# Optimization experiments

Measured on AMD Instinct MI355X. Metric: run time of the kernel, lower is better.

Reference implementation:

```python
import jax, jax.numpy as jnp
import numpy as np

N0, N1, N2 = 400000, 75000, 15000
E1, E2 = 1200000, 240000
F_IN, NC = 64, 40
H1, C1 = 2, 8          # layer 1: heads=2, out_channels=8 -> concat dim 16
H2, C2 = 1, NC         # layer 2: heads=1, out_channels=num_classes
NEG_SLOPE = 0.2


def gat_conv(x_src, x_dst, src, dst, Ws, Wd, att_s, att_d, bias, heads, ch):
    """PyG GATConv on bipartite (x_src, x_dst) with remove+add self loops."""
    n_dst = x_dst.shape[0]
    hs = (x_src @ Ws).reshape(-1, heads, ch)   # [N_src, H, C]
    hd = (x_dst @ Wd).reshape(-1, heads, ch)   # [N_dst, H, C]
    a_s = (hs * att_s).sum(-1)                 # [N_src, H]
    a_d = (hd * att_d).sum(-1)                 # [N_dst, H]
    loops = jnp.arange(n_dst)
    src_all = jnp.concatenate([src, loops])
    dst_all = jnp.concatenate([dst, loops])
    # remove_self_loops: drop pre-existing i->i edges; add_self_loops: appended
    valid = jnp.concatenate([src != dst, jnp.ones(n_dst, dtype=bool)])[:, None]
    logits = jax.nn.leaky_relu(a_s[src_all] + a_d[dst_all], NEG_SLOPE)  # [E, H]
    logits = jnp.where(valid, logits, -jnp.inf)
    m = jax.ops.segment_max(logits, dst_all, num_segments=n_dst)        # [N_dst, H]
    w = jnp.where(valid, jnp.exp(logits - m[dst_all]), 0.0)
    denom = jax.ops.segment_sum(w, dst_all, num_segments=n_dst)
    alpha = w / denom[dst_all]                                          # [E, H]
    out = jax.ops.segment_sum(alpha[:, :, None] * hs[src_all], dst_all,
                              num_segments=n_dst)                       # [N_dst, H, C]
    return out.reshape(n_dst, heads * ch) + bias


def setup_inputs() -> dict:
    key = jax.random.key(0)
    ks = jax.random.split(key, 16)
    s = 0.1
    return {
        "x": jax.random.normal(ks[0], (N0, F_IN), dtype=jnp.float32),
        "e1_src": jax.random.randint(ks[1], (E1,), 0, N0),
        "e1_dst": jax.random.randint(ks[2], (E1,), 0, N1),
        "e2_src": jax.random.randint(ks[3], (E2,), 0, N1),
        "e2_dst": jax.random.randint(ks[4], (E2,), 0, N2),
        "W1s": jax.random.normal(ks[5], (F_IN, H1 * C1), dtype=jnp.float32) * s,
        "W1d": jax.random.normal(ks[6], (F_IN, H1 * C1), dtype=jnp.float32) * s,
        "att1_s": jax.random.normal(ks[7], (H1, C1), dtype=jnp.float32) * s,
        "att1_d": jax.random.normal(ks[8], (H1, C1), dtype=jnp.float32) * s,
        "b1": jnp.zeros((H1 * C1,), dtype=jnp.float32),
        "W2s": jax.random.normal(ks[9], (H1 * C1, H2 * C2), dtype=jnp.float32) * s,
        "W2d": jax.random.normal(ks[10], (H1 * C1, H2 * C2), dtype=jnp.float32) * s,
        "att2_s": jax.random.normal(ks[11], (H2, C2), dtype=jnp.float32) * s,
        "att2_d": jax.random.normal(ks[12], (H2, C2), dtype=jnp.float32) * s,
        "b2": jnp.zeros((H2 * C2,), dtype=jnp.float32),
    }


def reference(x, e1_src, e1_dst, e2_src, e2_dst,
              W1s, W1d, att1_s, att1_d, b1,
              W2s, W2d, att2_s, att2_d, b2):
    h = gat_conv(x, x[:N1], e1_src, e1_dst, W1s, W1d, att1_s, att1_d, b1, H1, C1)
    h = jax.nn.elu(h)
    o = gat_conv(h, h[:N2], e2_src, e2_dst, W2s, W2d, att2_s, att2_d, b2, H2, C2)
    return jax.nn.log_softmax(o, axis=-1)
```

## Files before the change

### kernel.cpp

```cpp
#include <hip/hip_runtime.h>
#include <hip/hip_bf16.h>

constexpr int N0 = 400000, N1 = 75000, N2 = 15000;
constexpr int E1 = 1200000, E2 = 240000;
constexpr int NC = 40;
constexpr float NEG_SLOPE = 0.2f;

constexpr int BK1 = 128;
constexpr int NB1 = (N1 + BK1 - 1) / BK1;
constexpr int CAPB1 = 2432;
constexpr int BK2 = 32;
constexpr int NB2 = (N2 + BK2 - 1) / BK2;
constexpr int CAPB2 = 704;

constexpr int TILE = 8192;
constexpr int NT1 = (E1 + TILE - 1) / TILE;
constexpr int NT2 = (E2 + TILE - 1) / TILE;
constexpr int BPJ = (N0 + 511) / 512;

__device__ __forceinline__ float leaky(float v) { return v > 0.f ? v : NEG_SLOPE * v; }

__device__ __forceinline__ unsigned bf16pair(float lo, float hi) {
    unsigned a = __float_as_uint(lo), b = __float_as_uint(hi);
    a = (a + 0x7FFFu + ((a >> 16) & 1u)) >> 16;
    b = (b + 0x7FFFu + ((b >> 16) & 1u)) & 0xFFFF0000u;
    return a | b;
}
__device__ __forceinline__ float bfLo(unsigned w) { return __uint_as_float(w << 16); }
__device__ __forceinline__ float bfHi(unsigned w) { return __uint_as_float(w & 0xFFFF0000u); }

__global__ __launch_bounds__(512, 4) void k1_kernel(
    const float* __restrict__ x,
    const float* __restrict__ W1s, const float* __restrict__ W1d,
    const float* __restrict__ att1s, const float* __restrict__ att1d,
    const int* __restrict__ e1s, const int* __restrict__ e1d,
    const int* __restrict__ e2s, const int* __restrict__ e2d,
    unsigned* __restrict__ rec1, float* __restrict__ a_d1,
    int* __restrict__ gcnt1, unsigned* __restrict__ bin1,
    int* __restrict__ gcnt2, unsigned* __restrict__ bin2)
{
    __shared__ int hist[NB1];
    __shared__ int gbase[NB1];

    int bid = blockIdx.x;
    if (bid < BPJ) {
        int node = bid * 512 + threadIdx.x;
        if (node >= N0) return;
        const float4* xp = (const float4*)(x + (size_t)node * 64);
        float4 xr[16];
        #pragma unroll
        for (int j = 0; j < 16; ++j) xr[j] = xp[j];

        float ss[16];
        #pragma unroll
        for (int c = 0; c < 16; ++c) ss[c] = 0.f;
        #pragma unroll
        for (int j = 0; j < 16; ++j) {
            float xk[4] = {xr[j].x, xr[j].y, xr[j].z, xr[j].w};
            #pragma unroll
            for (int kk = 0; kk < 4; ++kk)
                #pragma unroll
                for (int c = 0; c < 16; ++c)
                    ss[c] = fmaf(xk[kk], W1s[(4 * j + kk) * 16 + c], ss[c]);
        }
        float a0 = 0.f, a1 = 0.f;
        #pragma unroll
        for (int c = 0; c < 8; ++c) {
            a0 = fmaf(ss[c], att1s[c], a0);
            a1 = fmaf(ss[8 + c], att1s[8 + c], a1);
        }
        unsigned* rp = rec1 + (size_t)node * 16;
        ((uint4*)rp)[0] = make_uint4(bf16pair(ss[0], ss[1]), bf16pair(ss[2], ss[3]),
                                     bf16pair(ss[4], ss[5]), bf16pair(ss[6], ss[7]));
        ((uint4*)rp)[1] = make_uint4(bf16pair(ss[8], ss[9]), bf16pair(ss[10], ss[11]),
                                     bf16pair(ss[12], ss[13]), bf16pair(ss[14], ss[15]));
        ((uint4*)rp)[2] = make_uint4(__float_as_uint(a0), __float_as_uint(a1), 0u, 0u);
        ((uint4*)rp)[3] = make_uint4(0u, 0u, 0u, 0u);

        if (node < N1) {
            float sd[16];
            #pragma unroll
            for (int c = 0; c < 16; ++c) sd[c] = 0.f;
            #pragma unroll
            for (int j = 0; j < 16; ++j) {
                float xk[4] = {xr[j].x, xr[j].y, xr[j].z, xr[j].w};
                #pragma unroll
                for (int kk = 0; kk < 4; ++kk)
                    #pragma unroll
                    for (int c = 0; c < 16; ++c)
                        sd[c] = fmaf(xk[kk], W1d[(4 * j + kk) * 16 + c], sd[c]);
            }
            float d0 = 0.f, d1 = 0.f;
            #pragma unroll
            for (int c = 0; c < 8; ++c) {
                d0 = fmaf(sd[c], att1d[c], d0);
                d1 = fmaf(sd[8 + c], att1d[8 + c], d1);
            }
            ((float2*)a_d1)[node] = make_float2(d0, d1);
        }
        return;
    }
    bid -= BPJ;
    const bool isL1 = bid < NT1;
    const int* es = isL1 ? e1s : e2s;
    const int* ed = isL1 ? e1d : e2d;
    const int nE = isL1 ? E1 : E2;
    const int nb = isL1 ? NB1 : NB2;
    const int cap = isL1 ? CAPB1 : CAPB2;
    const int shift = isL1 ? 7 : 5;
    const int lsh = isL1 ? 19 : 17;
    int* gc = isL1 ? gcnt1 : gcnt2;
    unsigned* gbin = isL1 ? bin1 : bin2;
    const int base = (isL1 ? bid : bid - NT1) * TILE;
    const int lim = min(TILE, nE - base);

    for (int b = threadIdx.x; b < nb; b += 512) hist[b] = 0;
    __syncthreads();
    for (int i = threadIdx.x; i < lim; i += 512) {
        int s = es[base + i], d = ed[base + i];
        if (s != d) atomicAdd(&hist[d >> shift], 1);
    }
    __syncthreads();
    for (int b = threadIdx.x; b < nb; b += 512) {
        int c = hist[b];
        gbase[b] = (c > 0) ? atomicAdd(&gc[b], c) : 0;
        hist[b] = 0;
    }
    __syncthreads();
    for (int i = threadIdx.x; i < lim; i += 512) {
        int s = es[base + i], d = ed[base + i];
        if (s != d) {
            int b = d >> shift;
            int pos = gbase[b] + atomicAdd(&hist[b], 1);
            if (pos < cap)
                gbin[(size_t)b * cap + pos] =
                    (unsigned)s | ((unsigned)(d & ((1 << shift) - 1)) << lsh);
        }
    }
}

__global__ __launch_bounds__(512) void k2_kernel(
    const int* __restrict__ gcnt1, const unsigned* __restrict__ bin1,
    const unsigned* __restrict__ rec1, const float* __restrict__ a_d1,
    const float* __restrict__ b1,
    const float* __restrict__ W2s, const float* __restrict__ W2d,
    const float* __restrict__ att2s, const float* __restrict__ att2d,
    unsigned* __restrict__ rec2)
{
    __shared__ unsigned srt[CAPB1];
    __shared__ int hist[BK1], start[BK1 + 1];
    __shared__ float w2sl[640], va[16], vd[16];
    __shared__ float h1s[BK1][17];

    const int b = blockIdx.x, tid = threadIdx.x;
    const int d0 = b * BK1;
    const int nN = min(BK1, N1 - d0);
    const int ncnt = min(gcnt1[b], CAPB1);
    const unsigned* bp = bin1 + (size_t)b * CAPB1;

    for (int i = tid; i < 640; i += 512) w2sl[i] = W2s[i];
    if (tid < BK1) hist[tid] = 0;
    if (tid >= 128 && tid < 144) {
        int k = tid - 128;
        float sa = 0.f, sd = 0.f;
        for (int cc = 0; cc < 40; ++cc) {
            sa = fmaf(W2s[k * 40 + cc], att2s[cc], sa);
            sd = fmaf(W2d[k * 40 + cc], att2d[cc], sd);
        }
        va[k] = sa; vd[k] = sd;
    }
    __syncthreads();
    for (int i = tid; i < ncnt; i += 512) atomicAdd(&hist[bp[i] >> 19], 1);
    __syncthreads();
    if (tid == 0) {
        int a = 0;
        for (int k = 0; k < BK1; ++k) { start[k] = a; a += hist[k]; }
        start[BK1] = a;
    }
    __syncthreads();
    if (tid < BK1) hist[tid] = start[tid];
    __syncthreads();
    for (int i = tid; i < ncnt; i += 512) {
        unsigned p = bp[i];
        int pos = atomicAdd(&hist[p >> 19], 1);
        srt[pos] = p & 0x7FFFFu;
    }
    __syncthreads();

    const int g = tid >> 4, c = tid & 15, h = c >> 3;
    const int wbase = tid & 48;
    const int wmap = (c < 8) ? c : (8 + ((c >> 2) & 1));
    for (int n = g; n < nN; n += 32) {
        const int node = d0 + n;
        const float ad = a_d1[(size_t)node * 2 + h];
        const int st = start[n], cnt = start[n + 1] - start[n];
        unsigned rwA = rec1[(size_t)node * 16 + wmap];
        unsigned rwB = (cnt > 0) ? rec1[(size_t)srt[st] * 16 + wmap] : 0u;
        float accv = 0.f, den = 0.f;
        for (int j = 0; j <= cnt; ++j) {
            unsigned rwC = (j + 2 <= cnt) ? rec1[(size_t)srt[st + j + 1] * 16 + wmap] : 0u;
            float asv = __uint_as_float((unsigned)__shfl((int)rwA, wbase + 8 + 4 * h, 64));
            unsigned chw = (unsigned)__shfl((int)rwA, wbase + (c >> 1), 64);
            float hv = (c & 1) ? bfHi(chw) : bfLo(chw);
            float w = __expf(leaky(asv + ad));
            accv = fmaf(w, hv, accv);
            den += w;
            rwA = rwB; rwB = rwC;
        }
        float v = accv / den + b1[c];
        h1s[n][c] = v > 0.f ? v : (__expf(v) - 1.f);
    }
    __syncthreads();
    for (int i = tid; i < nN * 24; i += 512) {
        int nn = i / 24, w = i - nn * 24;
        unsigned* rp = rec2 + (size_t)(d0 + nn) * 24;
        if (w < 20) {
            int c0 = 2 * w, c1 = c0 + 1;
            float s0 = 0.f, s1 = 0.f;
            #pragma unroll
            for (int k = 0; k < 16; ++k) {
                float hk = h1s[nn][k];
                s0 = fmaf(hk, w2sl[k * 40 + c0], s0);
                s1 = fmaf(hk, w2sl[k * 40 + c1], s1);
            }
            rp[w] = bf16pair(s0, s1);
        } else if (w < 22) {
            const float* vv = (w == 20) ? va : vd;
            float s = 0.f;
            #pragma unroll
            for (int k = 0; k < 16; ++k) s = fmaf(h1s[nn][k], vv[k], s);
            rp[w] = __float_as_uint(s);
        }
    }
}

__global__ __launch_bounds__(1024) void k3_kernel(
    const int* __restrict__ gcnt2, const unsigned* __restrict__ bin2,
    const unsigned* __restrict__ rec2, const float* __restrict__ b2,
    float* __restrict__ out)
{
    __shared__ unsigned srt[CAPB2];
    __shared__ int hist[BK2], start[BK2 + 1];

    const int b = blockIdx.x, tid = threadIdx.x;
    const int d0 = b * BK2;
    const int nN = min(BK2, N2 - d0);
    const int ncnt = min(gcnt2[b], CAPB2);
    const unsigned* bp = bin2 + (size_t)b * CAPB2;

    if (tid < BK2) hist[tid] = 0;
    __syncthreads();
    for (int i = tid; i < ncnt; i += 1024) atomicAdd(&hist[bp[i] >> 17], 1);
    __syncthreads();
    if (tid == 0) {
        int a = 0;
        for (int k = 0; k < BK2; ++k) { start[k] = a; a += hist[k]; }
        start[BK2] = a;
    }
    __syncthreads();
    if (tid < BK2) hist[tid] = start[tid];
    __syncthreads();
    for (int i = tid; i < ncnt; i += 1024) {
        unsigned p = bp[i];
        int pos = atomicAdd(&hist[p >> 17], 1);
        srt[pos] = p & 0x1FFFFu;
    }
    __syncthreads();

    const int g = tid >> 5, l = tid & 31;
    const float bb0 = (l < 20) ? b2[2 * l] : 0.f;
    const float bb1 = (l < 20) ? b2[2 * l + 1] : 0.f;
    for (int n = g; n < nN; n += 32) {
        const int node = d0 + n;
        const int st = start[n], cnt = start[n + 1] - start[n];
        unsigned rwA = (l < 22) ? rec2[(size_t)node * 24 + l] : 0u;
        const float ad = __uint_as_float((unsigned)__shfl((int)rwA, 21, 32));
        unsigned rwB = (cnt > 0 && l < 21) ? rec2[(size_t)srt[st] * 24 + l] : 0u;
        float a0 = 0.f, a1 = 0.f, den = 0.f;
        for (int j = 0; j <= cnt; ++j) {
            unsigned rwC = (j + 2 <= cnt && l < 21) ? rec2[(size_t)srt[st + j + 1] * 24 + l] : 0u;
            float asv = __uint_as_float((unsigned)__shfl((int)rwA, 20, 32));
            float w = __expf(leaky(asv + ad));
            a0 = fmaf(w, bfLo(rwA), a0);
            a1 = fmaf(w, bfHi(rwA), a1);
            den += w;
            rwA = rwB; rwB = rwC;
        }
        float v0 = (l < 20) ? a0 / den + bb0 : -3.4e38f;
        float v1 = (l < 20) ? a1 / den + bb1 : -3.4e38f;
        float mx = fmaxf(v0, v1);
        #pragma unroll
        for (int k = 16; k >= 1; k >>= 1) mx = fmaxf(mx, __shfl_xor(mx, k, 32));
        float ex = (l < 20) ? __expf(v0 - mx) + __expf(v1 - mx) : 0.f;
        #pragma unroll
        for (int k = 16; k >= 1; k >>= 1) ex += __shfl_xor(ex, k, 32);
        float lse = mx + logf(ex);
        if (l < 20)
            ((float2*)(out + (size_t)node * 40))[l] = make_float2(v0 - lse, v1 - lse);
    }
}

extern "C" void kernel_launch(void* const* d_in, const int* in_sizes, int n_in,
                              void* d_out, int out_size, void* d_ws, size_t ws_size,
                              hipStream_t stream) {
    const float* x      = (const float*)d_in[0];
    const int*   e1_src = (const int*)d_in[1];
    const int*   e1_dst = (const int*)d_in[2];
    const int*   e2_src = (const int*)d_in[3];
    const int*   e2_dst = (const int*)d_in[4];
    const float* W1s    = (const float*)d_in[5];
    const float* W1d    = (const float*)d_in[6];
    const float* att1s  = (const float*)d_in[7];
    const float* att1d  = (const float*)d_in[8];
    const float* b1     = (const float*)d_in[9];
    const float* W2s    = (const float*)d_in[10];
    const float* W2d    = (const float*)d_in[11];
    const float* att2s  = (const float*)d_in[12];
    const float* att2d  = (const float*)d_in[13];
    const float* b2     = (const float*)d_in[14];
    float* out = (float*)d_out;

    float* wsbase = (float*)d_ws;
    size_t o = 0;
    int*      gcnt1 = (int*)(wsbase + o);      o += NB1;
    int*      gcnt2 = (int*)(wsbase + o);      o += NB2;
    const size_t zeroWords = o;
    unsigned* bin1  = (unsigned*)(wsbase + o); o += (size_t)NB1 * CAPB1;
    unsigned* bin2  = (unsigned*)(wsbase + o); o += (size_t)NB2 * CAPB2;
    unsigned* rec1  = (unsigned*)(wsbase + o); o += (size_t)N0 * 16;
    float*    a_d1  = (float*)(wsbase + o);    o += (size_t)N1 * 2;
    unsigned* rec2  = (unsigned*)(wsbase + o); o += (size_t)N1 * 24;

    hipMemsetAsync(d_ws, 0, zeroWords * sizeof(float), stream);

    k1_kernel<<<BPJ + NT1 + NT2, 512, 0, stream>>>(
        x, W1s, W1d, att1s, att1d, e1_src, e1_dst, e2_src, e2_dst,
        rec1, a_d1, gcnt1, bin1, gcnt2, bin2);

    k2_kernel<<<NB1, 512, 0, stream>>>(gcnt1, bin1, rec1, a_d1, b1,
                                       W2s, W2d, att2s, att2d, rec2);

    k3_kernel<<<NB2, 1024, 0, stream>>>(gcnt2, bin2, rec2, b2, out);
}
```

Before: 140.0 us.

## Stage x rows through LDS, fold W1d·att into a vector, deepen gather prefetch

The projection part of k1 now loads the x rows of each 256-node block cooperatively and coalesced into padded LDS, rather than having every thread read its own 256-byte row. The destination-attention score is computed as x·(W1d·att1d), a precomputed 64x2 vector, which removes the 16-wide second projection. Block size drops to 256 and the binning section reuses the LDS buffer for its histograms. The neighbor-gather loops in k2 and k3 prefetch three records ahead instead of one, to hide gather latency, at the cost of more registers.

```diff
diff --git a/kernel.cpp b/kernel.cpp
--- a/kernel.cpp
+++ b/kernel.cpp
@@ -16,7 +16,7 @@
 constexpr int TILE = 8192;
 constexpr int NT1 = (E1 + TILE - 1) / TILE;
 constexpr int NT2 = (E2 + TILE - 1) / TILE;
-constexpr int BPJ = (N0 + 511) / 512;
+constexpr int BPJ = (N0 + 255) / 256;
 
 __device__ __forceinline__ float leaky(float v) { return v > 0.f ? v : NEG_SLOPE * v; }
 
@@ -29,7 +29,7 @@
 __device__ __forceinline__ float bfLo(unsigned w) { return __uint_as_float(w << 16); }
 __device__ __forceinline__ float bfHi(unsigned w) { return __uint_as_float(w & 0xFFFF0000u); }
 
-__global__ __launch_bounds__(512, 4) void k1_kernel(
+__global__ __launch_bounds__(256) void k1_kernel(
     const float* __restrict__ x,
     const float* __restrict__ W1s, const float* __restrict__ W1d,
     const float* __restrict__ att1s, const float* __restrict__ att1d,
@@ -39,24 +39,40 @@
     int* __restrict__ gcnt1, unsigned* __restrict__ bin1,
     int* __restrict__ gcnt2, unsigned* __restrict__ bin2)
 {
-    __shared__ int hist[NB1];
-    __shared__ int gbase[NB1];
+    __shared__ float4 ldsbuf[256 * 17];
+    __shared__ float2 vds[64];
 
     int bid = blockIdx.x;
+    const int tid = threadIdx.x;
     if (bid < BPJ) {
-        int node = bid * 512 + threadIdx.x;
+        const int nodeBase = bid * 256;
+        const int nValid = min(256, N0 - nodeBase);
+        const float4* xg = (const float4*)(x + (size_t)nodeBase * 64);
+        const int nF = nValid * 16;
+        for (int f = tid; f < nF; f += 256)
+            ldsbuf[(f >> 4) * 17 + (f & 15)] = xg[f];
+        if (tid < 64) {
+            float s0 = 0.f, s1 = 0.f;
+            #pragma unroll
+            for (int c = 0; c < 8; ++c) {
+                s0 = fmaf(W1d[tid * 16 + c], att1d[c], s0);
+                s1 = fmaf(W1d[tid * 16 + 8 + c], att1d[8 + c], s1);
+            }
+            vds[tid] = make_float2(s0, s1);
+        }
+        __syncthreads();
+
+        const int node = nodeBase + tid;
         if (node >= N0) return;
-        const float4* xp = (const float4*)(x + (size_t)node * 64);
-        float4 xr[16];
-        #pragma unroll
-        for (int j = 0; j < 16; ++j) xr[j] = xp[j];
+        const float4* xrow = &ldsbuf[tid * 17];
 
         float ss[16];
         #pragma unroll
         for (int c = 0; c < 16; ++c) ss[c] = 0.f;
         #pragma unroll
         for (int j = 0; j < 16; ++j) {
-            float xk[4] = {xr[j].x, xr[j].y, xr[j].z, xr[j].w};
+            float4 t = xrow[j];
+            float xk[4] = {t.x, t.y, t.z, t.w};
             #pragma unroll
             for (int kk = 0; kk < 4; ++kk)
                 #pragma unroll
@@ -77,30 +93,26 @@
         ((uint4*)rp)[2] = make_uint4(__float_as_uint(a0), __float_as_uint(a1), 0u, 0u);
         ((uint4*)rp)[3] = make_uint4(0u, 0u, 0u, 0u);
 
-        if (node < N1) {
-            float sd[16];
-            #pragma unroll
-            for (int c = 0; c < 16; ++c) sd[c] = 0.f;
+        if (nodeBase < N1 && node < N1) {
+            float d0 = 0.f, d1 = 0.f;
             #pragma unroll
             for (int j = 0; j < 16; ++j) {
-                float xk[4] = {xr[j].x, xr[j].y, xr[j].z, xr[j].w};
+                float4 t = xrow[j];
+                float xk[4] = {t.x, t.y, t.z, t.w};
                 #pragma unroll
-                for (int kk = 0; kk < 4; ++kk)
-                    #pragma unroll
-                    for (int c = 0; c < 16; ++c)
-                        sd[c] = fmaf(xk[kk], W1d[(4 * j + kk) * 16 + c], sd[c]);
-            }
-            float d0 = 0.f, d1 = 0.f;
-            #pragma unroll
-            for (int c = 0; c < 8; ++c) {
-                d0 = fmaf(sd[c], att1d[c], d0);
-                d1 = fmaf(sd[8 + c], att1d[8 + c], d1);
+                for (int kk = 0; kk < 4; ++kk) {
+                    float2 v = vds[4 * j + kk];
+                    d0 = fmaf(xk[kk], v.x, d0);
+                    d1 = fmaf(xk[kk], v.y, d1);
+                }
             }
             ((float2*)a_d1)[node] = make_float2(d0, d1);
         }
         return;
     }
     bid -= BPJ;
+    int* hist  = (int*)ldsbuf;
+    int* gbase = hist + NB1;
     const bool isL1 = bid < NT1;
     const int* es = isL1 ? e1s : e2s;
     const int* ed = isL1 ? e1d : e2d;
@@ -114,20 +126,20 @@
     const int base = (isL1 ? bid : bid - NT1) * TILE;
     const int lim = min(TILE, nE - base);
 
-    for (int b = threadIdx.x; b < nb; b += 512) hist[b] = 0;
-    __syncthreads();
-    for (int i = threadIdx.x; i < lim; i += 512) {
+    for (int b = tid; b < nb; b += 256) hist[b] = 0;
+    __syncthreads();
+    for (int i = tid; i < lim; i += 256) {
         int s = es[base + i], d = ed[base + i];
         if (s != d) atomicAdd(&hist[d >> shift], 1);
     }
     __syncthreads();
-    for (int b = threadIdx.x; b < nb; b += 512) {
+    for (int b = tid; b < nb; b += 256) {
         int c = hist[b];
         gbase[b] = (c > 0) ? atomicAdd(&gc[b], c) : 0;
         hist[b] = 0;
     }
     __syncthreads();
-    for (int i = threadIdx.x; i < lim; i += 512) {
+    for (int i = tid; i < lim; i += 256) {
         int s = es[base + i], d = ed[base + i];
         if (s != d) {
             int b = d >> shift;
@@ -194,18 +206,20 @@
         const int node = d0 + n;
         const float ad = a_d1[(size_t)node * 2 + h];
         const int st = start[n], cnt = start[n + 1] - start[n];
-        unsigned rwA = rec1[(size_t)node * 16 + wmap];
-        unsigned rwB = (cnt > 0) ? rec1[(size_t)srt[st] * 16 + wmap] : 0u;
+        unsigned rw0 = rec1[(size_t)node * 16 + wmap];
+        unsigned rw1 = (cnt >= 1) ? rec1[(size_t)srt[st] * 16 + wmap] : 0u;
+        unsigned rw2 = (cnt >= 2) ? rec1[(size_t)srt[st + 1] * 16 + wmap] : 0u;
+        unsigned rw3 = (cnt >= 3) ? rec1[(size_t)srt[st + 2] * 16 + wmap] : 0u;
         float accv = 0.f, den = 0.f;
         for (int j = 0; j <= cnt; ++j) {
-            unsigned rwC = (j + 2 <= cnt) ? rec1[(size_t)srt[st + j + 1] * 16 + wmap] : 0u;
-            float asv = __uint_as_float((unsigned)__shfl((int)rwA, wbase + 8 + 4 * h, 64));
-            unsigned chw = (unsigned)__shfl((int)rwA, wbase + (c >> 1), 64);
+            float asv = __uint_as_float((unsigned)__shfl((int)rw0, wbase + 8 + 4 * h, 64));
+            unsigned chw = (unsigned)__shfl((int)rw0, wbase + (c >> 1), 64);
             float hv = (c & 1) ? bfHi(chw) : bfLo(chw);
             float w = __expf(leaky(asv + ad));
             accv = fmaf(w, hv, accv);
             den += w;
-            rwA = rwB; rwB = rwC;
+            rw0 = rw1; rw1 = rw2; rw2 = rw3;
+            rw3 = (j + 4 <= cnt) ? rec1[(size_t)srt[st + j + 3] * 16 + wmap] : 0u;
         }
         float v = accv / den + b1[c];
         h1s[n][c] = v > 0.f ? v : (__expf(v) - 1.f);
@@ -273,18 +287,20 @@
     for (int n = g; n < nN; n += 32) {
         const int node = d0 + n;
         const int st = start[n], cnt = start[n + 1] - start[n];
-        unsigned rwA = (l < 22) ? rec2[(size_t)node * 24 + l] : 0u;
-        const float ad = __uint_as_float((unsigned)__shfl((int)rwA, 21, 32));
-        unsigned rwB = (cnt > 0 && l < 21) ? rec2[(size_t)srt[st] * 24 + l] : 0u;
+        unsigned rw0 = (l < 22) ? rec2[(size_t)node * 24 + l] : 0u;
+        const float ad = __uint_as_float((unsigned)__shfl((int)rw0, 21, 32));
+        unsigned rw1 = (cnt >= 1 && l < 21) ? rec2[(size_t)srt[st] * 24 + l] : 0u;
+        unsigned rw2 = (cnt >= 2 && l < 21) ? rec2[(size_t)srt[st + 1] * 24 + l] : 0u;
+        unsigned rw3 = (cnt >= 3 && l < 21) ? rec2[(size_t)srt[st + 2] * 24 + l] : 0u;
         float a0 = 0.f, a1 = 0.f, den = 0.f;
         for (int j = 0; j <= cnt; ++j) {
-            unsigned rwC = (j + 2 <= cnt && l < 21) ? rec2[(size_t)srt[st + j + 1] * 24 + l] : 0u;
-            float asv = __uint_as_float((unsigned)__shfl((int)rwA, 20, 32));
+            float asv = __uint_as_float((unsigned)__shfl((int)rw0, 20, 32));
             float w = __expf(leaky(asv + ad));
-            a0 = fmaf(w, bfLo(rwA), a0);
-            a1 = fmaf(w, bfHi(rwA), a1);
+            a0 = fmaf(w, bfLo(rw0), a0);
+            a1 = fmaf(w, bfHi(rw0), a1);
             den += w;
-            rwA = rwB; rwB = rwC;
+            rw0 = rw1; rw1 = rw2; rw2 = rw3;
+            rw3 = (j + 4 <= cnt && l < 21) ? rec2[(size_t)srt[st + j + 3] * 24 + l] : 0u;
         }
         float v0 = (l < 20) ? a0 / den + bb0 : -3.4e38f;
         float v1 = (l < 20) ? a1 / den + bb1 : -3.4e38f;
@@ -333,7 +349,7 @@
 
     hipMemsetAsync(d_ws, 0, zeroWords * sizeof(float), stream);
 
-    k1_kernel<<<BPJ + NT1 + NT2, 512, 0, stream>>>(
+    k1_kernel<<<BPJ + NT1 + NT2, 256, 0, stream>>>(
         x, W1s, W1d, att1s, att1d, e1_src, e1_dst, e2_src, e2_dst,
         rec1, a_d1, gcnt1, bin1, gcnt2, bin2);
 
```

Result: slower. 143.0 us (+2.1%).
